# Optimization experiments

Hardware: AMD Instinct MI355X
Metric: run time of the kernel (lower is better)

The kernel has to match this reference:

```python
import jax, jax.numpy as jnp
import numpy as np

B, L, D_MODEL = 2, 2048, 1024
D_STATE, D_CONV, EXPAND = 8, 4, 2
D_INNER = EXPAND * D_MODEL          # 2048
DT_RANK = (D_MODEL + 15) // 16      # 64


def setup_inputs() -> dict:
    key = jax.random.key(0)
    ks = jax.random.split(key, 8)
    s = 0.02
    x = jax.random.normal(ks[0], (B, L, D_MODEL), dtype=jnp.float32)
    W_in = jax.random.normal(ks[1], (D_MODEL, 2 * D_INNER), dtype=jnp.float32) * s
    dw_kernel = jax.random.normal(ks[2], (D_CONV, D_INNER), dtype=jnp.float32) * s  # depthwise
    pw_kernel = jax.random.normal(ks[3], (D_INNER, D_INNER), dtype=jnp.float32) * s  # pointwise
    conv_bias = jnp.zeros((D_INNER,), dtype=jnp.float32)
    W_x = jax.random.normal(ks[4], (D_INNER, DT_RANK + 2 * D_STATE), dtype=jnp.float32) * s
    W_dt = jax.random.normal(ks[5], (DT_RANK, D_INNER), dtype=jnp.float32) * s
    b_dt = jnp.zeros((D_INNER,), dtype=jnp.float32)
    # A = repeat(range(1..d_state), d_inner).reshape(d_inner, d_state), stored as log
    A_init = np.repeat(np.arange(1, D_STATE + 1, dtype=np.float32), D_INNER).reshape(D_INNER, D_STATE)
    A_log = jnp.asarray(np.log(A_init))
    D = jnp.ones((D_INNER,), dtype=jnp.float32)
    W_out = jax.random.normal(ks[6], (D_INNER, D_MODEL), dtype=jnp.float32) * s
    return {"x": x, "W_in": W_in, "dw_kernel": dw_kernel, "pw_kernel": pw_kernel,
            "conv_bias": conv_bias, "W_x": W_x, "W_dt": W_dt, "b_dt": b_dt,
            "A_log": A_log, "D": D, "W_out": W_out}


def reference(x, W_in, dw_kernel, pw_kernel, conv_bias, W_x, W_dt, b_dt, A_log, D, W_out):
    d_inner, d_state = A_log.shape
    dt_rank = W_dt.shape[0]
    d_conv = dw_kernel.shape[0]
    bsz = x.shape[0]

    xz = x @ W_in                                   # [B,L,2*di]
    x_in, z = jnp.split(xz, 2, axis=-1)             # each [B,L,di]

    # causal separable conv: depthwise (causal pad) -> pointwise -> swish
    xp = jnp.pad(x_in, ((0, 0), (d_conv - 1, 0), (0, 0)))
    xc = jax.lax.conv_general_dilated(
        xp, dw_kernel[:, None, :], window_strides=(1,), padding='VALID',
        dimension_numbers=('NWC', 'WIO', 'NWC'), feature_group_count=d_inner)
    xc = jax.nn.silu(xc @ pw_kernel + conv_bias)    # [B,L,di]

    x_dbl = xc @ W_x                                # [B,L,dt_rank+2*ds]
    delta = x_dbl[..., :dt_rank]
    Bm = x_dbl[..., dt_rank:dt_rank + d_state]      # [B,L,ds]
    C = x_dbl[..., dt_rank + d_state:]              # [B,L,ds]
    delta = jax.nn.softplus(delta @ W_dt + b_dt)    # [B,L,di]

    A = -jnp.exp(A_log)                             # [di,ds]
    deltaA = jnp.exp(jnp.einsum('bld,dn->bldn', delta, A))       # [B,L,di,ds]
    deltaB_u = jnp.einsum('bld,bln,bld->bldn', delta, Bm, xc)    # [B,L,di,ds]

    def step(h, inp):
        dA_t, dBu_t, C_t = inp
        h = dA_t * h + dBu_t                        # [B,di,ds]
        y_t = jnp.einsum('bn,bdn->bd', C_t, h)      # [B,di]
        return h, y_t

    h0 = jnp.zeros((bsz, d_inner, d_state), dtype=x.dtype)
    elems = (deltaA.transpose(1, 0, 2, 3), deltaB_u.transpose(1, 0, 2, 3), C.transpose(1, 0, 2))
    _, ys = jax.lax.scan(step, h0, elems)           # ys: [L,B,di]
    y = ys.transpose(1, 0, 2)                       # [B,L,di]

    y = y + xc * D
    y = y * jax.nn.silu(z)
    return y @ W_out                                # [B,L,d_model]
```

## Files before the change

kernel.cpp:

```cpp
#include <hip/hip_runtime.h>
#include <math.h>

#define Bb 2
#define Ll 2048
#define DMODEL 1024
#define DINNER 2048
#define DSTATE 8
#define DTRANK 64
#define DCONV 4
#define MM (Bb*Ll)
#define NCH 64
#define CL 32
#define G3_KCH 8
#define G3_KC (DINNER / G3_KCH)

typedef __attribute__((ext_vector_type(8))) short    bf16x8;
typedef __attribute__((ext_vector_type(4))) float    f32x4;

__device__ __forceinline__ float silu_f(float x) {
    return x / (1.0f + __expf(-x));
}
__device__ __forceinline__ float softplus_f(float x) {
    return fmaxf(x, 0.0f) + log1pf(__expf(-fabsf(x)));
}
__device__ __forceinline__ unsigned short f2bf(float f) {
    unsigned int u = __float_as_uint(f);
    u += 0x7fffu + ((u >> 16) & 1u);
    return (unsigned short)(u >> 16);
}
__device__ __forceinline__ float bf2f(unsigned short u) {
    return __uint_as_float(((unsigned int)u) << 16);
}
__device__ __forceinline__ void async_cp16(const unsigned short* g, unsigned short* l) {
    __builtin_amdgcn_global_load_lds(
        (const __attribute__((address_space(1))) void*)g,
        (__attribute__((address_space(3))) void*)l, 16, 0, 0);
}

template <int EPI, int TN, typename OT>
__global__ __launch_bounds__(256, 4) void mfma_gemm(
    const unsigned short* __restrict__ A, const unsigned short* __restrict__ Bt,
    OT* __restrict__ C, OT* __restrict__ C2, int nsplit, size_t czstride,
    int M, int N, int K, int lda, int ldb, int ldc,
    const float* __restrict__ bias)
{
    constexpr int NJ = TN / 32;
    __shared__ unsigned short As[2][128 * 32];
    __shared__ unsigned short Bs[2][TN * 32];

    const int bm = blockIdx.y * 128;
    const int bn = blockIdx.x * TN;
    const int tid  = threadIdx.x;
    const int w    = tid >> 6;
    const int lane = tid & 63;
    const int wm = (w >> 1) * 64;
    const int wn = (w & 1) * (TN / 2);
    const int lr = lane & 15;
    const int lq = lane >> 4;

    const size_t kz = (size_t)blockIdx.z * K;
    A  += kz;
    Bt += kz;
    C  += (size_t)blockIdx.z * czstride;

    const int row  = tid >> 2;
    const int sp   = tid & 3;
    const int slog = sp ^ ((row >> 1) & 3);
    const unsigned short* gA1 = A  + (size_t)(bm + row) * lda + slog * 8;
    const unsigned short* gA2 = gA1 + (size_t)64 * lda;
    const unsigned short* gB1 = Bt + (size_t)(bn + row) * ldb + slog * 8;
    const unsigned short* gB2 = gB1 + (size_t)64 * ldb;
    const int st = tid * 8;

    const int fsw = (lq ^ ((lr >> 1) & 3)) * 8;

    f32x4 acc[4][NJ];
#pragma unroll
    for (int i = 0; i < 4; ++i)
#pragma unroll
        for (int j = 0; j < NJ; ++j) acc[i][j] = (f32x4){0.f, 0.f, 0.f, 0.f};

    async_cp16(gA1, &As[0][st]);
    async_cp16(gA2, &As[0][2048 + st]);
    async_cp16(gB1, &Bs[0][st]);
    if (TN == 128) async_cp16(gB2, &Bs[0][2048 + st]);

    int cur = 0;
    for (int k0 = 0; k0 < K; k0 += 32, cur ^= 1) {
        __syncthreads();
        const int nk = k0 + 32;
        if (nk < K) {
            const int nb = cur ^ 1;
            async_cp16(gA1 + nk, &As[nb][st]);
            async_cp16(gA2 + nk, &As[nb][2048 + st]);
            async_cp16(gB1 + nk, &Bs[nb][st]);
            if (TN == 128) async_cp16(gB2 + nk, &Bs[nb][2048 + st]);
        }

        bf16x8 a[4], b[NJ];
#pragma unroll
        for (int i = 0; i < 4; ++i)
            a[i] = *(const bf16x8*)&As[cur][(wm + i * 16 + lr) * 32 + fsw];
#pragma unroll
        for (int j = 0; j < NJ; ++j)
            b[j] = *(const bf16x8*)&Bs[cur][(wn + j * 16 + lr) * 32 + fsw];
#pragma unroll
        for (int i = 0; i < 4; ++i)
#pragma unroll
            for (int j = 0; j < NJ; ++j)
                acc[i][j] = __builtin_amdgcn_mfma_f32_16x16x32_bf16(
                    a[i], b[j], acc[i][j], 0, 0, 0);
    }

#pragma unroll
    for (int i = 0; i < 4; ++i) {
        const int row0 = bm + wm + i * 16 + lq * 4;
#pragma unroll
        for (int j = 0; j < NJ; ++j) {
            const int col = bn + wn + j * 16 + lr;
            OT* Cb; int colb;
            if (col < nsplit) { Cb = C; colb = col; }
            else              { Cb = C2; colb = col - nsplit; }
            float bv = (EPI == 1) ? bias[col] : 0.0f;
#pragma unroll
            for (int r = 0; r < 4; ++r) {
                float v = acc[i][j][r];
                if (EPI == 1) v = silu_f(v + bv);
                if (sizeof(OT) == 2)
                    Cb[(size_t)(row0 + r) * ldc + colb] = (OT)f2bf(v);
                else
                    Cb[(size_t)(row0 + r) * ldc + colb] = (OT)v;
            }
        }
    }
}

__global__ __launch_bounds__(256) void g5_reduce(
    const float* __restrict__ part, float* __restrict__ out, int n)
{
    int i = (blockIdx.x * 256 + threadIdx.x) * 4;
    if (i >= n) return;
    float4 a = *(const float4*)&part[i];
    float4 b = *(const float4*)&part[(size_t)n + i];
    a.x += b.x; a.y += b.y; a.z += b.z; a.w += b.w;
    *(float4*)&out[i] = a;
}

__global__ __launch_bounds__(256) void gemm_tiled_sp(
    const float* __restrict__ A, const float* __restrict__ B,
    float* __restrict__ C, int M, int N, int K,
    int lda, int ldb, int ldc, const float* __restrict__ bias)
{
    __shared__ float As[16][68];
    __shared__ float Bs[16][68];

    const int bm = blockIdx.y * 64;
    const int bn = blockIdx.x * 64;
    const int tid = threadIdx.x;
    const int tx = tid & 15;
    const int ty = tid >> 4;

    float acc[4][4];
#pragma unroll
    for (int i = 0; i < 4; ++i)
#pragma unroll
        for (int j = 0; j < 4; ++j) acc[i][j] = 0.0f;

    const int ar = tid >> 2;
    const int ac = (tid & 3) << 2;
    const int br = tid >> 4;
    const int bc = (tid & 15) << 2;

    for (int k0 = 0; k0 < K; k0 += 16) {
        float4 av = *(const float4*)&A[(size_t)(bm + ar) * lda + k0 + ac];
        float4 bv = *(const float4*)&B[(size_t)(k0 + br) * ldb + bn + bc];
        As[ac + 0][ar] = av.x;
        As[ac + 1][ar] = av.y;
        As[ac + 2][ar] = av.z;
        As[ac + 3][ar] = av.w;
        *(float4*)&Bs[br][bc] = bv;
        __syncthreads();
#pragma unroll
        for (int k = 0; k < 16; ++k) {
            float4 a4 = *(float4*)&As[k][ty * 4];
            float4 b4 = *(float4*)&Bs[k][tx * 4];
            float am[4] = {a4.x, a4.y, a4.z, a4.w};
            float bn4[4] = {b4.x, b4.y, b4.z, b4.w};
#pragma unroll
            for (int i = 0; i < 4; ++i)
#pragma unroll
                for (int j = 0; j < 4; ++j)
                    acc[i][j] = fmaf(am[i], bn4[j], acc[i][j]);
        }
        __syncthreads();
    }

    const int col = bn + tx * 4;
#pragma unroll
    for (int i = 0; i < 4; ++i) {
        int row = bm + ty * 4 + i;
        float4 v = make_float4(acc[i][0], acc[i][1], acc[i][2], acc[i][3]);
        v.x = softplus_f(v.x + bias[col + 0]);
        v.y = softplus_f(v.y + bias[col + 1]);
        v.z = softplus_f(v.z + bias[col + 2]);
        v.w = softplus_f(v.w + bias[col + 3]);
        *(float4*)&C[(size_t)row * ldc + col] = v;
    }
}

__global__ __launch_bounds__(256) void g3_splitk(
    const unsigned short* __restrict__ xc, const float* __restrict__ Wx,
    float* __restrict__ part)
{
    __shared__ float As[16][68];
    __shared__ float Bs[16][85];
    const int m0 = blockIdx.x * 64;
    const int kb = blockIdx.y * G3_KC;
    const int t = threadIdx.x;
    const int tr = t >> 4;
    const int tc = t & 15;

    const int arow = t >> 2;
    const int ak4  = (t & 3) * 4;
    const int bk   = t >> 4;
    const int bc   = (t & 15) * 5;

    float acc[4][5];
#pragma unroll
    for (int r = 0; r < 4; ++r)
#pragma unroll
        for (int c = 0; c < 5; ++c) acc[r][c] = 0.0f;

    for (int k0 = 0; k0 < G3_KC; k0 += 16) {
        ushort4 av = *(const ushort4*)&xc[(size_t)(m0 + arow) * DINNER + kb + k0 + ak4];
        float bv[5];
#pragma unroll
        for (int q = 0; q < 5; ++q)
            bv[q] = Wx[(size_t)(kb + k0 + bk) * 80 + bc + q];
        __syncthreads();
        As[ak4 + 0][arow] = bf2f(av.x);
        As[ak4 + 1][arow] = bf2f(av.y);
        As[ak4 + 2][arow] = bf2f(av.z);
        As[ak4 + 3][arow] = bf2f(av.w);
#pragma unroll
        for (int q = 0; q < 5; ++q) Bs[bk][bc + q] = bv[q];
        __syncthreads();
#pragma unroll
        for (int k = 0; k < 16; ++k) {
            float a[4], b[5];
#pragma unroll
            for (int r = 0; r < 4; ++r) a[r] = As[k][tr * 4 + r];
#pragma unroll
            for (int c = 0; c < 5; ++c) b[c] = Bs[k][tc * 5 + c];
#pragma unroll
            for (int r = 0; r < 4; ++r)
#pragma unroll
                for (int c = 0; c < 5; ++c)
                    acc[r][c] = fmaf(a[r], b[c], acc[r][c]);
        }
    }
#pragma unroll
    for (int r = 0; r < 4; ++r)
#pragma unroll
        for (int c = 0; c < 5; ++c)
            part[((size_t)blockIdx.y * MM + m0 + tr * 4 + r) * 80 + tc * 5 + c] = acc[r][c];
}

__global__ __launch_bounds__(256) void g3_reduce(
    const float* __restrict__ part, float* __restrict__ xdbl)
{
    int i = (blockIdx.x * 256 + threadIdx.x) * 4;
    if (i >= MM * 80) return;
    float4 s = *(const float4*)&part[i];
#pragma unroll
    for (int c = 1; c < G3_KCH; ++c) {
        float4 p = *(const float4*)&part[(size_t)c * MM * 80 + i];
        s.x += p.x; s.y += p.y; s.z += p.z; s.w += p.w;
    }
    *(float4*)&xdbl[i] = s;
}

__global__ __launch_bounds__(256) void transpose_cast(
    const float* __restrict__ src, unsigned short* __restrict__ dst, int R, int C)
{
    __shared__ float tile[32][33];
    const int c0 = blockIdx.x * 32;
    const int r0 = blockIdx.y * 32;
    const int tx = threadIdx.x;
    const int ty = threadIdx.y;
#pragma unroll
    for (int i = 0; i < 32; i += 8)
        tile[ty + i][tx] = src[(size_t)(r0 + ty + i) * C + c0 + tx];
    __syncthreads();
#pragma unroll
    for (int i = 0; i < 32; i += 8)
        dst[(size_t)(c0 + ty + i) * R + r0 + tx] = f2bf(tile[tx][ty + i]);
}

__global__ __launch_bounds__(256) void cast_bf16(
    const float* __restrict__ src, unsigned short* __restrict__ dst, int n)
{
    int i = (blockIdx.x * 256 + threadIdx.x) * 4;
    if (i >= n) return;
    float4 v = *(const float4*)&src[i];
    ushort4 o;
    o.x = f2bf(v.x); o.y = f2bf(v.y); o.z = f2bf(v.z); o.w = f2bf(v.w);
    *(ushort4*)&dst[i] = o;
}

__global__ __launch_bounds__(256) void dwconv_kernel(
    const unsigned short* __restrict__ x_in, const float* __restrict__ dwk,
    unsigned short* __restrict__ out)
{
    int i4 = blockIdx.x * 256 + threadIdx.x;
    if (i4 >= MM * DINNER / 4) return;
    int d = (i4 * 4) & (DINNER - 1);
    int bl = (i4 * 4) >> 11;
    int l = bl & (Ll - 1);
    int b = bl >> 11;
    float a0 = 0.f, a1 = 0.f, a2 = 0.f, a3 = 0.f;
#pragma unroll
    for (int k = 0; k < DCONV; ++k) {
        int t = l + k - (DCONV - 1);
        if (t >= 0) {
            ushort4 xv = *(const ushort4*)&x_in[(size_t)(b * Ll + t) * DINNER + d];
            float4 wv = *(const float4*)&dwk[k * DINNER + d];
            a0 = fmaf(bf2f(xv.x), wv.x, a0);
            a1 = fmaf(bf2f(xv.y), wv.y, a1);
            a2 = fmaf(bf2f(xv.z), wv.z, a2);
            a3 = fmaf(bf2f(xv.w), wv.w, a3);
        }
    }
    ushort4 o;
    o.x = f2bf(a0); o.y = f2bf(a1); o.z = f2bf(a2); o.w = f2bf(a3);
    *(ushort4*)&out[i4 * 4] = o;
}

__global__ __launch_bounds__(256) void scan_pass1(
    const float* __restrict__ delta, const unsigned short* __restrict__ xc,
    const float* __restrict__ xdbl, const float* __restrict__ A_log,
    float* __restrict__ cs_a, float* __restrict__ cs_h)
{
    const int d = blockIdx.x * 256 + threadIdx.x;
    const int c = blockIdx.y;
    const int b = blockIdx.z;
    const int t0 = c * CL;

    __shared__ float sB[CL][8];
    {
        int i = threadIdx.x;
        int t = i >> 3, j = i & 7;
        sB[t][j] = xdbl[((size_t)(b * Ll + t0 + t)) * 80 + DTRANK + j];
    }
    __syncthreads();

    float An[8];
#pragma unroll
    for (int n = 0; n < 8; ++n) An[n] = -__expf(A_log[d * 8 + n]);

    float h[8], ap[8];
#pragma unroll
    for (int n = 0; n < 8; ++n) { h[n] = 0.0f; ap[n] = 1.0f; }

    const float* dptr = delta + ((size_t)(b * Ll + t0)) * DINNER + d;
    const unsigned short* xptr = xc + ((size_t)(b * Ll + t0)) * DINNER + d;

#pragma unroll 4
    for (int t = 0; t < CL; ++t) {
        float dl = dptr[(size_t)t * DINNER];
        float xv = bf2f(xptr[(size_t)t * DINNER]);
        float du = dl * xv;
#pragma unroll
        for (int n = 0; n < 8; ++n) {
            float dA = __expf(dl * An[n]);
            h[n] = fmaf(dA, h[n], du * sB[t][n]);
            ap[n] *= dA;
        }
    }

    size_t base = (((size_t)(b * NCH + c)) * 8) * DINNER + d;
#pragma unroll
    for (int n = 0; n < 8; ++n) {
        cs_a[base + (size_t)n * DINNER] = ap[n];
        cs_h[base + (size_t)n * DINNER] = h[n];
    }
}

__global__ __launch_bounds__(256) void scan_pass2(
    const float* __restrict__ cs_a, const float* cs_h, float* hin)
{
    int idx = blockIdx.x * 256 + threadIdx.x;
    if (idx >= Bb * 8 * DINNER) return;
    int d = idx & (DINNER - 1);
    int n = (idx >> 11) & 7;
    int b = idx >> 14;
    float H = 0.0f;
#pragma unroll 4
    for (int c = 0; c < NCH; ++c) {
        size_t o = (((size_t)(b * NCH + c)) * 8 + n) * DINNER + d;
        float a = cs_a[o];
        float hh = cs_h[o];
        hin[o] = H;
        H = fmaf(a, H, hh);
    }
}

__global__ __launch_bounds__(256) void scan_pass3(
    const float* __restrict__ delta, const unsigned short* __restrict__ xc,
    const float* __restrict__ xdbl, const float* __restrict__ A_log,
    const float* __restrict__ hin, const unsigned short* __restrict__ z,
    const float* __restrict__ Dvec, unsigned short* __restrict__ y_bf)
{
    const int d = blockIdx.x * 256 + threadIdx.x;
    const int c = blockIdx.y;
    const int b = blockIdx.z;
    const int t0 = c * CL;

    __shared__ float sB[CL][8];
    __shared__ float sC[CL][8];
    {
        int i = threadIdx.x;
        int t = i >> 4, j = i & 15;
        float v = xdbl[((size_t)(b * Ll + t0 + t)) * 80 + DTRANK + j];
        if (j < 8) sB[t][j] = v; else sC[t][j - 8] = v;
        t = (i + 256) >> 4; j = (i + 256) & 15;
        v = xdbl[((size_t)(b * Ll + t0 + t)) * 80 + DTRANK + j];
        if (j < 8) sB[t][j] = v; else sC[t][j - 8] = v;
    }
    __syncthreads();

    float An[8];
#pragma unroll
    for (int n = 0; n < 8; ++n) An[n] = -__expf(A_log[d * 8 + n]);

    float h[8];
    size_t hbase = (((size_t)(b * NCH + c)) * 8) * DINNER + d;
#pragma unroll
    for (int n = 0; n < 8; ++n) h[n] = hin[hbase + (size_t)n * DINNER];

    const float Dd = Dvec[d];
    const float* dptr = delta + ((size_t)(b * Ll + t0)) * DINNER + d;
    const unsigned short* xptr = xc + ((size_t)(b * Ll + t0)) * DINNER + d;
    const unsigned short* zptr = z + ((size_t)(b * Ll + t0)) * DINNER + d;
    unsigned short* yptr = y_bf + ((size_t)(b * Ll + t0)) * DINNER + d;

    for (int t = 0; t < CL; ++t) {
        float dl = dptr[(size_t)t * DINNER];
        float xv = bf2f(xptr[(size_t)t * DINNER]);
        float du = dl * xv;
        float yt = 0.0f;
#pragma unroll
        for (int n = 0; n < 8; ++n) {
            float dA = __expf(dl * An[n]);
            h[n] = fmaf(dA, h[n], du * sB[t][n]);
            yt = fmaf(sC[t][n], h[n], yt);
        }
        float zv = bf2f(zptr[(size_t)t * DINNER]);
        yptr[(size_t)t * DINNER] = f2bf((yt + xv * Dd) * silu_f(zv));
    }
}

extern "C" void kernel_launch(void* const* d_in, const int* in_sizes, int n_in,
                              void* d_out, int out_size, void* d_ws, size_t ws_size,
                              hipStream_t stream)
{
    const float* x         = (const float*)d_in[0];
    const float* W_in      = (const float*)d_in[1];
    const float* dwk       = (const float*)d_in[2];
    const float* pwk       = (const float*)d_in[3];
    const float* conv_bias = (const float*)d_in[4];
    const float* W_x       = (const float*)d_in[5];
    const float* W_dt      = (const float*)d_in[6];
    const float* b_dt      = (const float*)d_in[7];
    const float* A_log     = (const float*)d_in[8];
    const float* Dv        = (const float*)d_in[9];
    const float* W_out     = (const float*)d_in[10];
    float* out = (float*)d_out;

    char* ws = (char*)d_ws;
    unsigned short* x_in_bf = (unsigned short*)(ws);
    unsigned short* z_bf    = (unsigned short*)(ws + (16ull << 20));
    float*          delta   = (float*)(ws + (32ull << 20));
    float*          g5part  = (float*)(ws + (32ull << 20));
    unsigned short* x_bf    = (unsigned short*)(ws + (64ull << 20));
    unsigned short* y_bf    = (unsigned short*)(ws + (64ull << 20));
    unsigned short* Wint    = (unsigned short*)(ws + (72ull << 20));
    unsigned short* pw_t    = (unsigned short*)(ws + (80ull << 20));
    unsigned short* xcp_bf  = (unsigned short*)(ws + (88ull << 20));
    unsigned short* xc_bf   = (unsigned short*)(ws + (104ull << 20));
    unsigned short* Woutt   = (unsigned short*)(ws + (120ull << 20));
    float*          xdbl    = (float*)(ws + (124ull << 20));
    float*          g3part  = (float*)(ws + (126ull << 20));
    float*          cs_a    = (float*)(ws + (136ull << 20));
    float*          cs_h    = (float*)(ws + (144ull << 20));
    float*          hin     = cs_h;

    dim3 blk(256);

    cast_bf16<<<(MM * DMODEL / 4 + 255) / 256, blk, 0, stream>>>(x, x_bf, MM * DMODEL);
    transpose_cast<<<dim3((2 * DINNER) / 32, DMODEL / 32), dim3(32, 8), 0, stream>>>(
        W_in, Wint, DMODEL, 2 * DINNER);
    transpose_cast<<<dim3(DINNER / 32, DINNER / 32), dim3(32, 8), 0, stream>>>(
        pwk, pw_t, DINNER, DINNER);
    transpose_cast<<<dim3(DMODEL / 32, DINNER / 32), dim3(32, 8), 0, stream>>>(
        W_out, Woutt, DINNER, DMODEL);

    mfma_gemm<0, 128, unsigned short><<<dim3((2 * DINNER) / 128, MM / 128, 1), blk, 0, stream>>>(
        x_bf, Wint, x_in_bf, z_bf, DINNER, 0,
        MM, 2 * DINNER, DMODEL, DMODEL, DMODEL, DINNER, nullptr);

    dwconv_kernel<<<MM * DINNER / 4 / 256, blk, 0, stream>>>(x_in_bf, dwk, xcp_bf);

    mfma_gemm<1, 64, unsigned short><<<dim3(DINNER / 64, MM / 128, 1), blk, 0, stream>>>(
        xcp_bf, pw_t, xc_bf, xc_bf, DINNER + 1, 0,
        MM, DINNER, DINNER, DINNER, DINNER, DINNER, conv_bias);

    g3_splitk<<<dim3(MM / 64, G3_KCH), blk, 0, stream>>>(xc_bf, W_x, g3part);
    g3_reduce<<<(MM * 80 / 4 + 255) / 256, blk, 0, stream>>>(g3part, xdbl);

    gemm_tiled_sp<<<dim3(DINNER / 64, MM / 64), blk, 0, stream>>>(
        xdbl, W_dt, delta, MM, DINNER, DTRANK, 80, DINNER, DINNER, b_dt);

    scan_pass1<<<dim3(DINNER / 256, NCH, Bb), blk, 0, stream>>>(
        delta, xc_bf, xdbl, A_log, cs_a, cs_h);
    scan_pass2<<<(Bb * 8 * DINNER + 255) / 256, blk, 0, stream>>>(cs_a, cs_h, hin);
    scan_pass3<<<dim3(DINNER / 256, NCH, Bb), blk, 0, stream>>>(
        delta, xc_bf, xdbl, A_log, hin, z_bf, Dv, y_bf);

    mfma_gemm<0, 64, float><<<dim3(DMODEL / 64, MM / 128, 2), blk, 0, stream>>>(
        y_bf, Woutt, g5part, g5part, DMODEL + 1, (size_t)MM * DMODEL,
        MM, DMODEL, DINNER / 2, DINNER, DINNER, DMODEL, nullptr);
    g5_reduce<<<(MM * DMODEL / 4 + 255) / 256, blk, 0, stream>>>(
        g5part, out, MM * DMODEL);
}
```

Measured before the change: 401.5 us.

## Fuse prep kernels, fold split-K reductions into consumers, retile MFMA GEMMs

Merges the input cast and three weight transpose-casts into one prep launch. Removes the g3_reduce and g5_reduce kernels: the W_dt GEMM and both scan passes now sum the split-K partials directly, and the output GEMM runs full K with no split. Generalises the MFMA GEMM to a variable wave count so the pointwise GEMM can use 512-thread blocks with 128-wide N tiles. The aim is fewer launches and less intermediate traffic. The cost is duplicated partial-sum reads in several consumers and less parallelism in the output GEMM.

```diff
diff --git a/kernel.cpp b/kernel.cpp
--- a/kernel.cpp
+++ b/kernel.cpp
@@ -37,14 +37,21 @@
         (__attribute__((address_space(3))) void*)l, 16, 0, 0);
 }
 
-template <int EPI, int TN, typename OT>
-__global__ __launch_bounds__(256, 4) void mfma_gemm(
+template <int EPI, int NW, int TN, typename OT>
+__global__ __launch_bounds__(NW * 64, 4) void mfma_gemm(
     const unsigned short* __restrict__ A, const unsigned short* __restrict__ Bt,
-    OT* __restrict__ C, OT* __restrict__ C2, int nsplit, size_t czstride,
+    OT* __restrict__ C, OT* __restrict__ C2, int nsplit,
     int M, int N, int K, int lda, int ldb, int ldc,
     const float* __restrict__ bias)
 {
-    constexpr int NJ = TN / 32;
+    constexpr int NT   = NW * 64;
+    constexpr int WNC  = NW / 2;
+    constexpr int WNE  = TN / WNC;
+    constexpr int NJ   = WNE / 16;
+    constexpr int RPP  = NT / 4;
+    constexpr int APASS = 128 / RPP;
+    constexpr int BPASS = TN / RPP;
+
     __shared__ unsigned short As[2][128 * 32];
     __shared__ unsigned short Bs[2][TN * 32];
 
@@ -53,23 +60,16 @@
     const int tid  = threadIdx.x;
     const int w    = tid >> 6;
     const int lane = tid & 63;
-    const int wm = (w >> 1) * 64;
-    const int wn = (w & 1) * (TN / 2);
+    const int wm = (w / WNC) * 64;
+    const int wn = (w % WNC) * WNE;
     const int lr = lane & 15;
     const int lq = lane >> 4;
-
-    const size_t kz = (size_t)blockIdx.z * K;
-    A  += kz;
-    Bt += kz;
-    C  += (size_t)blockIdx.z * czstride;
 
     const int row  = tid >> 2;
     const int sp   = tid & 3;
     const int slog = sp ^ ((row >> 1) & 3);
-    const unsigned short* gA1 = A  + (size_t)(bm + row) * lda + slog * 8;
-    const unsigned short* gA2 = gA1 + (size_t)64 * lda;
-    const unsigned short* gB1 = Bt + (size_t)(bn + row) * ldb + slog * 8;
-    const unsigned short* gB2 = gB1 + (size_t)64 * ldb;
+    const unsigned short* gA = A  + (size_t)(bm + row) * lda + slog * 8;
+    const unsigned short* gB = Bt + (size_t)(bn + row) * ldb + slog * 8;
     const int st = tid * 8;
 
     const int fsw = (lq ^ ((lr >> 1) & 3)) * 8;
@@ -80,10 +80,12 @@
 #pragma unroll
         for (int j = 0; j < NJ; ++j) acc[i][j] = (f32x4){0.f, 0.f, 0.f, 0.f};
 
-    async_cp16(gA1, &As[0][st]);
-    async_cp16(gA2, &As[0][2048 + st]);
-    async_cp16(gB1, &Bs[0][st]);
-    if (TN == 128) async_cp16(gB2, &Bs[0][2048 + st]);
+#pragma unroll
+    for (int p = 0; p < APASS; ++p)
+        async_cp16(gA + (size_t)p * RPP * lda, &As[0][p * RPP * 32 + st]);
+#pragma unroll
+    for (int p = 0; p < BPASS; ++p)
+        async_cp16(gB + (size_t)p * RPP * ldb, &Bs[0][p * RPP * 32 + st]);
 
     int cur = 0;
     for (int k0 = 0; k0 < K; k0 += 32, cur ^= 1) {
@@ -91,10 +93,12 @@
         const int nk = k0 + 32;
         if (nk < K) {
             const int nb = cur ^ 1;
-            async_cp16(gA1 + nk, &As[nb][st]);
-            async_cp16(gA2 + nk, &As[nb][2048 + st]);
-            async_cp16(gB1 + nk, &Bs[nb][st]);
-            if (TN == 128) async_cp16(gB2 + nk, &Bs[nb][2048 + st]);
+#pragma unroll
+            for (int p = 0; p < APASS; ++p)
+                async_cp16(gA + (size_t)p * RPP * lda + nk, &As[nb][p * RPP * 32 + st]);
+#pragma unroll
+            for (int p = 0; p < BPASS; ++p)
+                async_cp16(gB + (size_t)p * RPP * ldb + nk, &Bs[nb][p * RPP * 32 + st]);
         }
 
         bf16x8 a[4], b[NJ];
@@ -135,21 +139,48 @@
     }
 }
 
-__global__ __launch_bounds__(256) void g5_reduce(
-    const float* __restrict__ part, float* __restrict__ out, int n)
-{
-    int i = (blockIdx.x * 256 + threadIdx.x) * 4;
-    if (i >= n) return;
-    float4 a = *(const float4*)&part[i];
-    float4 b = *(const float4*)&part[(size_t)n + i];
-    a.x += b.x; a.y += b.y; a.z += b.z; a.w += b.w;
-    *(float4*)&out[i] = a;
-}
-
-__global__ __launch_bounds__(256) void gemm_tiled_sp(
-    const float* __restrict__ A, const float* __restrict__ B,
-    float* __restrict__ C, int M, int N, int K,
-    int lda, int ldb, int ldc, const float* __restrict__ bias)
+__global__ __launch_bounds__(256) void prep_all(
+    const float* __restrict__ x, const float* __restrict__ W_in,
+    const float* __restrict__ pwk, const float* __restrict__ W_out,
+    unsigned short* __restrict__ x_bf, unsigned short* __restrict__ Wint,
+    unsigned short* __restrict__ pw_t, unsigned short* __restrict__ Woutt)
+{
+    const int b = blockIdx.x;
+    const int t = threadIdx.x;
+    if (b < 4096) {
+        int i = b * 1024 + t * 4;
+        float4 v = *(const float4*)&x[i];
+        ushort4 o;
+        o.x = f2bf(v.x); o.y = f2bf(v.y); o.z = f2bf(v.z); o.w = f2bf(v.w);
+        *(ushort4*)&x_bf[i] = o;
+        return;
+    }
+    const float* src; unsigned short* dst; int R, C, c0, r0;
+    if (b < 8192) {
+        int bi = b - 4096; src = W_in; dst = Wint; R = 1024; C = 4096;
+        c0 = (bi & 127) * 32; r0 = (bi >> 7) * 32;
+    } else if (b < 12288) {
+        int bi = b - 8192; src = pwk; dst = pw_t; R = 2048; C = 2048;
+        c0 = (bi & 63) * 32; r0 = (bi >> 6) * 32;
+    } else {
+        int bi = b - 12288; src = W_out; dst = Woutt; R = 2048; C = 1024;
+        c0 = (bi & 31) * 32; r0 = (bi >> 5) * 32;
+    }
+    __shared__ float tile[32][33];
+    const int tx = t & 31;
+    const int ty = t >> 5;
+#pragma unroll
+    for (int i = 0; i < 32; i += 8)
+        tile[ty + i][tx] = src[(size_t)(r0 + ty + i) * C + c0 + tx];
+    __syncthreads();
+#pragma unroll
+    for (int i = 0; i < 32; i += 8)
+        dst[(size_t)(c0 + ty + i) * R + r0 + tx] = f2bf(tile[tx][ty + i]);
+}
+
+__global__ __launch_bounds__(256) void g4_fused(
+    const float* __restrict__ part, const float* __restrict__ B,
+    float* __restrict__ C, const float* __restrict__ bias)
 {
     __shared__ float As[16][68];
     __shared__ float Bs[16][68];
@@ -171,9 +202,15 @@
     const int br = tid >> 4;
     const int bc = (tid & 15) << 2;
 
-    for (int k0 = 0; k0 < K; k0 += 16) {
-        float4 av = *(const float4*)&A[(size_t)(bm + ar) * lda + k0 + ac];
-        float4 bv = *(const float4*)&B[(size_t)(k0 + br) * ldb + bn + bc];
+    for (int k0 = 0; k0 < DTRANK; k0 += 16) {
+        float4 av = make_float4(0.f, 0.f, 0.f, 0.f);
+        const float* ap = &part[(size_t)(bm + ar) * 80 + k0 + ac];
+#pragma unroll
+        for (int kc = 0; kc < G3_KCH; ++kc) {
+            float4 p = *(const float4*)&ap[(size_t)kc * MM * 80];
+            av.x += p.x; av.y += p.y; av.z += p.z; av.w += p.w;
+        }
+        float4 bv = *(const float4*)&B[(size_t)(k0 + br) * DINNER + bn + bc];
         As[ac + 0][ar] = av.x;
         As[ac + 1][ar] = av.y;
         As[ac + 2][ar] = av.z;
@@ -204,7 +241,7 @@
         v.y = softplus_f(v.y + bias[col + 1]);
         v.z = softplus_f(v.z + bias[col + 2]);
         v.w = softplus_f(v.w + bias[col + 3]);
-        *(float4*)&C[(size_t)row * ldc + col] = v;
+        *(float4*)&C[(size_t)row * DINNER + col] = v;
     }
 }
 
@@ -264,48 +301,6 @@
 #pragma unroll
         for (int c = 0; c < 5; ++c)
             part[((size_t)blockIdx.y * MM + m0 + tr * 4 + r) * 80 + tc * 5 + c] = acc[r][c];
-}
-
-__global__ __launch_bounds__(256) void g3_reduce(
-    const float* __restrict__ part, float* __restrict__ xdbl)
-{
-    int i = (blockIdx.x * 256 + threadIdx.x) * 4;
-    if (i >= MM * 80) return;
-    float4 s = *(const float4*)&part[i];
-#pragma unroll
-    for (int c = 1; c < G3_KCH; ++c) {
-        float4 p = *(const float4*)&part[(size_t)c * MM * 80 + i];
-        s.x += p.x; s.y += p.y; s.z += p.z; s.w += p.w;
-    }
-    *(float4*)&xdbl[i] = s;
-}
-
-__global__ __launch_bounds__(256) void transpose_cast(
-    const float* __restrict__ src, unsigned short* __restrict__ dst, int R, int C)
-{
-    __shared__ float tile[32][33];
-    const int c0 = blockIdx.x * 32;
-    const int r0 = blockIdx.y * 32;
-    const int tx = threadIdx.x;
-    const int ty = threadIdx.y;
-#pragma unroll
-    for (int i = 0; i < 32; i += 8)
-        tile[ty + i][tx] = src[(size_t)(r0 + ty + i) * C + c0 + tx];
-    __syncthreads();
-#pragma unroll
-    for (int i = 0; i < 32; i += 8)
-        dst[(size_t)(c0 + ty + i) * R + r0 + tx] = f2bf(tile[tx][ty + i]);
-}
-
-__global__ __launch_bounds__(256) void cast_bf16(
-    const float* __restrict__ src, unsigned short* __restrict__ dst, int n)
-{
-    int i = (blockIdx.x * 256 + threadIdx.x) * 4;
-    if (i >= n) return;
-    float4 v = *(const float4*)&src[i];
-    ushort4 o;
-    o.x = f2bf(v.x); o.y = f2bf(v.y); o.z = f2bf(v.z); o.w = f2bf(v.w);
-    *(ushort4*)&dst[i] = o;
 }
 
 __global__ __launch_bounds__(256) void dwconv_kernel(
@@ -338,7 +333,7 @@
 
 __global__ __launch_bounds__(256) void scan_pass1(
     const float* __restrict__ delta, const unsigned short* __restrict__ xc,
-    const float* __restrict__ xdbl, const float* __restrict__ A_log,
+    const float* __restrict__ part, const float* __restrict__ A_log,
     float* __restrict__ cs_a, float* __restrict__ cs_h)
 {
     const int d = blockIdx.x * 256 + threadIdx.x;
@@ -350,7 +345,12 @@
     {
         int i = threadIdx.x;
         int t = i >> 3, j = i & 7;
-        sB[t][j] = xdbl[((size_t)(b * Ll + t0 + t)) * 80 + DTRANK + j];
+        size_t o = ((size_t)(b * Ll + t0 + t)) * 80 + DTRANK + j;
+        float v = 0.0f;
+#pragma unroll
+        for (int kc = 0; kc < G3_KCH; ++kc)
+            v += part[(size_t)kc * MM * 80 + o];
+        sB[t][j] = v;
     }
     __syncthreads();
 
@@ -407,7 +407,7 @@
 
 __global__ __launch_bounds__(256) void scan_pass3(
     const float* __restrict__ delta, const unsigned short* __restrict__ xc,
-    const float* __restrict__ xdbl, const float* __restrict__ A_log,
+    const float* __restrict__ part, const float* __restrict__ A_log,
     const float* __restrict__ hin, const unsigned short* __restrict__ z,
     const float* __restrict__ Dvec, unsigned short* __restrict__ y_bf)
 {
@@ -420,12 +420,17 @@
     __shared__ float sC[CL][8];
     {
         int i = threadIdx.x;
-        int t = i >> 4, j = i & 15;
-        float v = xdbl[((size_t)(b * Ll + t0 + t)) * 80 + DTRANK + j];
-        if (j < 8) sB[t][j] = v; else sC[t][j - 8] = v;
-        t = (i + 256) >> 4; j = (i + 256) & 15;
-        v = xdbl[((size_t)(b * Ll + t0 + t)) * 80 + DTRANK + j];
-        if (j < 8) sB[t][j] = v; else sC[t][j - 8] = v;
+#pragma unroll
+        for (int half = 0; half < 2; ++half) {
+            int ii = i + half * 256;
+            int t = ii >> 4, j = ii & 15;
+            size_t o = ((size_t)(b * Ll + t0 + t)) * 80 + DTRANK + j;
+            float v = 0.0f;
+#pragma unroll
+            for (int kc = 0; kc < G3_KCH; ++kc)
+                v += part[(size_t)kc * MM * 80 + o];
+            if (j < 8) sB[t][j] = v; else sC[t][j - 8] = v;
+        }
     }
     __syncthreads();
 
@@ -481,7 +486,6 @@
     unsigned short* x_in_bf = (unsigned short*)(ws);
     unsigned short* z_bf    = (unsigned short*)(ws + (16ull << 20));
     float*          delta   = (float*)(ws + (32ull << 20));
-    float*          g5part  = (float*)(ws + (32ull << 20));
     unsigned short* x_bf    = (unsigned short*)(ws + (64ull << 20));
     unsigned short* y_bf    = (unsigned short*)(ws + (64ull << 20));
     unsigned short* Wint    = (unsigned short*)(ws + (72ull << 20));
@@ -489,47 +493,40 @@
     unsigned short* xcp_bf  = (unsigned short*)(ws + (88ull << 20));
     unsigned short* xc_bf   = (unsigned short*)(ws + (104ull << 20));
     unsigned short* Woutt   = (unsigned short*)(ws + (120ull << 20));
-    float*          xdbl    = (float*)(ws + (124ull << 20));
     float*          g3part  = (float*)(ws + (126ull << 20));
     float*          cs_a    = (float*)(ws + (136ull << 20));
     float*          cs_h    = (float*)(ws + (144ull << 20));
     float*          hin     = cs_h;
-
     dim3 blk(256);
 
-    cast_bf16<<<(MM * DMODEL / 4 + 255) / 256, blk, 0, stream>>>(x, x_bf, MM * DMODEL);
-    transpose_cast<<<dim3((2 * DINNER) / 32, DMODEL / 32), dim3(32, 8), 0, stream>>>(
-        W_in, Wint, DMODEL, 2 * DINNER);
-    transpose_cast<<<dim3(DINNER / 32, DINNER / 32), dim3(32, 8), 0, stream>>>(
-        pwk, pw_t, DINNER, DINNER);
-    transpose_cast<<<dim3(DMODEL / 32, DINNER / 32), dim3(32, 8), 0, stream>>>(
-        W_out, Woutt, DINNER, DMODEL);
-
-    mfma_gemm<0, 128, unsigned short><<<dim3((2 * DINNER) / 128, MM / 128, 1), blk, 0, stream>>>(
-        x_bf, Wint, x_in_bf, z_bf, DINNER, 0,
+    prep_all<<<14336, blk, 0, stream>>>(x, W_in, pwk, W_out,
+                                        x_bf, Wint, pw_t, Woutt);
+
+    mfma_gemm<0, 4, 128, unsigned short>
+        <<<dim3((2 * DINNER) / 128, MM / 128), blk, 0, stream>>>(
+        x_bf, Wint, x_in_bf, z_bf, DINNER,
         MM, 2 * DINNER, DMODEL, DMODEL, DMODEL, DINNER, nullptr);
 
     dwconv_kernel<<<MM * DINNER / 4 / 256, blk, 0, stream>>>(x_in_bf, dwk, xcp_bf);
 
-    mfma_gemm<1, 64, unsigned short><<<dim3(DINNER / 64, MM / 128, 1), blk, 0, stream>>>(
-        xcp_bf, pw_t, xc_bf, xc_bf, DINNER + 1, 0,
+    mfma_gemm<1, 8, 128, unsigned short>
+        <<<dim3(DINNER / 128, MM / 128), dim3(512), 0, stream>>>(
+        xcp_bf, pw_t, xc_bf, xc_bf, DINNER + 1,
         MM, DINNER, DINNER, DINNER, DINNER, DINNER, conv_bias);
 
     g3_splitk<<<dim3(MM / 64, G3_KCH), blk, 0, stream>>>(xc_bf, W_x, g3part);
-    g3_reduce<<<(MM * 80 / 4 + 255) / 256, blk, 0, stream>>>(g3part, xdbl);
-
-    gemm_tiled_sp<<<dim3(DINNER / 64, MM / 64), blk, 0, stream>>>(
-        xdbl, W_dt, delta, MM, DINNER, DTRANK, 80, DINNER, DINNER, b_dt);
+
+    g4_fused<<<dim3(DINNER / 64, MM / 64), blk, 0, stream>>>(
+        g3part, W_dt, delta, b_dt);
 
     scan_pass1<<<dim3(DINNER / 256, NCH, Bb), blk, 0, stream>>>(
-        delta, xc_bf, xdbl, A_log, cs_a, cs_h);
+        delta, xc_bf, g3part, A_log, cs_a, cs_h);
     scan_pass2<<<(Bb * 8 * DINNER + 255) / 256, blk, 0, stream>>>(cs_a, cs_h, hin);
     scan_pass3<<<dim3(DINNER / 256, NCH, Bb), blk, 0, stream>>>(
-        delta, xc_bf, xdbl, A_log, hin, z_bf, Dv, y_bf);
-
-    mfma_gemm<0, 64, float><<<dim3(DMODEL / 64, MM / 128, 2), blk, 0, stream>>>(
-        y_bf, Woutt, g5part, g5part, DMODEL + 1, (size_t)MM * DMODEL,
-        MM, DMODEL, DINNER / 2, DINNER, DINNER, DMODEL, nullptr);
-    g5_reduce<<<(MM * DMODEL / 4 + 255) / 256, blk, 0, stream>>>(
-        g5part, out, MM * DMODEL);
-}
+        delta, xc_bf, g3part, A_log, hin, z_bf, Dv, y_bf);
+
+    mfma_gemm<0, 4, 64, float>
+        <<<dim3(DMODEL / 64, MM / 128), blk, 0, stream>>>(
+        y_bf, Woutt, out, out, DMODEL + 1,
+        MM, DMODEL, DINNER, DINNER, DINNER, DMODEL, nullptr);
+}
```

New measurement: 381.8 us. -4.9%, faster.
